# Kernel optimization log

Hardware: AMD Instinct MI355X
Metric: run time of the kernel (lower is better)

## Reference

```python
import jax, jax.numpy as jnp
import numpy as np
from jax import lax

B, T1, T2, C = 8, 128, 128, 256
K = 3

def setup_inputs() -> dict:
    key = jax.random.key(0)
    k1, k2, kw, kb = jax.random.split(key, 4)
    x1 = jax.random.normal(k1, (B, T1, C), dtype=jnp.float32)
    x2 = jax.random.normal(k2, (B, T2, C), dtype=jnp.float32)
    # conv2d: in_channels = 2C, out_channels = C, kernel 3x3 (OIHW)
    fan_in = 2 * C * K * K
    bound = 1.0 / np.sqrt(fan_in)
    W = jax.random.uniform(kw, (C, 2 * C, K, K), jnp.float32, -bound, bound)
    b = jax.random.uniform(kb, (C,), jnp.float32, -bound, bound)
    alpha = jnp.float32(0.5)
    return {"x1": x1, "x2": x2, "W": W, "b": b, "alpha": alpha}


def reference(x1, x2, W, b, alpha):
    # x1: [B, T1, C], x2: [B, T2, C]
    a = jnp.transpose(x1, (0, 2, 1))  # [B, C, T1]
    c2 = jnp.transpose(x2, (0, 2, 1))  # [B, C, T2]
    Bd, Cd, T1d = a.shape
    T2d = c2.shape[-1]
    # joint outer-product tensor: [B, 2C, T1, T2]
    j1 = jnp.broadcast_to(a[:, :, :, None], (Bd, Cd, T1d, T2d))
    j2 = jnp.broadcast_to(c2[:, :, None, :], (Bd, Cd, T1d, T2d))
    joint = jnp.concatenate([j1, j2], axis=1)
    out = lax.conv_general_dilated(
        joint, W, window_strides=(1, 1), padding="SAME",
        dimension_numbers=("NCHW", "OIHW", "NCHW"))
    out = out + b[None, :, None, None]
    out = jax.nn.gelu(out, approximate=False)  # torch nn.GELU default = exact erf
    out_T1 = jnp.mean(out, axis=-1)            # [B, C, T1]
    out_T1 = jnp.transpose(out_T1, (0, 2, 1))  # [B, T1, C]
    return out_T1 * alpha + x1
```

## Files before the change

kernel.cpp:

```cpp
#include <hip/hip_runtime.h>
#include <math.h>

#define B_   8
#define T_   128
#define C_   256
#define KP   768
#define NQ   768

typedef unsigned short ushort;
typedef ushort ushort4v __attribute__((ext_vector_type(4)));
typedef ushort ushort8v __attribute__((ext_vector_type(8)));
typedef __bf16 bf16x8  __attribute__((ext_vector_type(8)));
typedef float  f32x4   __attribute__((ext_vector_type(4)));

__device__ __forceinline__ ushort f2bf(float f) {
    unsigned u = __float_as_uint(f);
    u += 0x7fffu + ((u >> 16) & 1u);
    return (ushort)(u >> 16);
}

__device__ __forceinline__ float gelu_fast(float x) {
    float x2 = x * x;
    float y  = x * fmaf(0.0713548162726f, x2, 1.59576912161f);
    float e  = __expf(-y);
    return x * __builtin_amdgcn_rcpf(1.0f + e);
}

__global__ __launch_bounds__(256) void tc_pack(
    const float* __restrict__ x1, const float* __restrict__ x2,
    const float* __restrict__ W, ushort* __restrict__ Lmat,
    ushort* __restrict__ Wmat)
{
    const int bid = blockIdx.x, tid = threadIdx.x;
    if (bid < 1536) {
        int cid  = bid * 256 + tid;
        int pc   = cid % 192;
        int rest = cid / 192;
        int m    = rest & 127;
        int sb   = rest >> 7;
        int tap  = pc >> 6, ci = (pc & 63) * 4;
        const float* X = (sb >= 8 ? x2 + (size_t)(sb - 8) * T_ * C_
                                  : x1 + (size_t)sb * T_ * C_);
        int row = m + tap - 1;
        float4 v = make_float4(0.f, 0.f, 0.f, 0.f);
        if (row >= 0 && row < T_) v = *(const float4*)&X[row * C_ + ci];
        ushort4v u; u.x = f2bf(v.x); u.y = f2bf(v.y); u.z = f2bf(v.z); u.w = f2bf(v.w);
        *(ushort4v*)&Lmat[(size_t)cid * 4] = u;
    } else {
        int cid  = (bid - 1536) * 256 + tid;
        int pc   = cid % 192;
        int rest = cid / 192;
        int q    = rest % 768;
        int s    = rest / 768;
        int tap  = pc >> 6, ci = (pc & 63) * 4;
        int o    = q / 3;
        int r    = q - o * 3;
        ushort4v u;
        #pragma unroll
        for (int j = 0; j < 4; ++j) {
            int cj = ci + j;
            int addr = (s == 0) ? o * 4608 + cj * 9 + tap * 3 + r
                                : o * 4608 + (256 + cj) * 9 + r * 3 + tap;
            float w = W[addr];
            ushort b = f2bf(w);
            if (j == 0) u.x = b; else if (j == 1) u.y = b; else if (j == 2) u.z = b; else u.w = b;
        }
        *(ushort4v*)&Wmat[(size_t)cid * 4] = u;
    }
}

__global__ __launch_bounds__(256) void tc_mfma(
    const ushort* __restrict__ Lmat, const ushort* __restrict__ Wmat,
    float* __restrict__ Y)
{
    const int tile_n = blockIdx.x;
    const int tile_m = blockIdx.y;
    const int side   = blockIdx.z & 1;
    const int b      = blockIdx.z >> 1;

    __shared__ ushort As[64 * 40];
    __shared__ ushort Bs[64 * 40];

    const int tid = threadIdx.x;
    const int l   = tid & 63, w = tid >> 6;
    const int wr  = w >> 1,  wc = w & 1;
    const int r16 = l & 15,  kb = l >> 4;

    f32x4 acc[2][2] = {};

    const ushort* Lbase = Lmat + ((size_t)(side * B_ + b) * T_ + tile_m * 64 + (tid >> 2)) * KP + (tid & 3) * 8;
    const ushort* Wbase = Wmat + ((size_t)side * NQ + tile_n * 64 + (tid >> 2)) * KP + (tid & 3) * 8;
    const int aoff = (tid >> 2) * 40 + (tid & 3) * 8;

    const int ra = (wr * 32 + r16) * 40 + kb * 8;
    const int rb = (wc * 32 + r16) * 40 + kb * 8;

    ushort8v av = *(const ushort8v*)Lbase;
    ushort8v bv = *(const ushort8v*)Wbase;

    for (int k0 = 0; k0 < KP; k0 += 32) {
        __syncthreads();
        *(ushort8v*)&As[aoff] = av;
        *(ushort8v*)&Bs[aoff] = bv;
        __syncthreads();
        if (k0 < KP - 32) {
            av = *(const ushort8v*)(Lbase + k0 + 32);
            bv = *(const ushort8v*)(Wbase + k0 + 32);
        }
        bf16x8 a0 = __builtin_bit_cast(bf16x8, *(const ushort8v*)&As[ra]);
        bf16x8 a1 = __builtin_bit_cast(bf16x8, *(const ushort8v*)&As[ra + 16 * 40]);
        bf16x8 b0 = __builtin_bit_cast(bf16x8, *(const ushort8v*)&Bs[rb]);
        bf16x8 b1 = __builtin_bit_cast(bf16x8, *(const ushort8v*)&Bs[rb + 16 * 40]);
        acc[0][0] = __builtin_amdgcn_mfma_f32_16x16x32_bf16(a0, b0, acc[0][0], 0, 0, 0);
        acc[0][1] = __builtin_amdgcn_mfma_f32_16x16x32_bf16(a0, b1, acc[0][1], 0, 0, 0);
        acc[1][0] = __builtin_amdgcn_mfma_f32_16x16x32_bf16(a1, b0, acc[1][0], 0, 0, 0);
        acc[1][1] = __builtin_amdgcn_mfma_f32_16x16x32_bf16(a1, b1, acc[1][1], 0, 0, 0);
    }

    #pragma unroll
    for (int j = 0; j < 2; ++j) {
        int gq = tile_n * 64 + wc * 32 + j * 16 + r16;
        #pragma unroll
        for (int i = 0; i < 2; ++i) {
            int gm = tile_m * 64 + wr * 32 + i * 16 + kb * 4;
            float* p = Y + ((size_t)(side * B_ + b) * NQ + gq) * T_ + gm;
            *(f32x4*)p = acc[i][j];
        }
    }
}

__global__ __launch_bounds__(128) void tc_finalize(
    const float* __restrict__ Y, const float* __restrict__ x1,
    const float* __restrict__ bias, const float* __restrict__ alpha_p,
    float* __restrict__ out)
{
    const int o = blockIdx.x & 255;
    const int b = blockIdx.x >> 8;
    const int t = threadIdx.x;

    __shared__ float Bs3[T_], BsT[T_], BsB[T_];

    const float* YB = Y + ((size_t)(B_ + b) * NQ + o * 3) * T_ + t;
    float b0 = YB[0], b1 = YB[T_], b2 = YB[2 * T_];
    Bs3[t] = b0 + b1 + b2;
    BsT[t] = b1 + b2;
    BsB[t] = b0 + b1;

    const float* YA = Y + ((size_t)b * NQ + o * 3) * T_ + t;
    float a0 = YA[0], a1 = YA[T_], a2 = YA[2 * T_];
    float bo = bias[o];
    float A3 = bo + a0 + a1 + a2;
    float Al = bo + a1 + a2;
    float Ar = bo + a0 + a1;

    __syncthreads();

    const float* Bsel = (t == 0) ? BsT : ((t == T_ - 1) ? BsB : Bs3);

    float s0 = 0.f, s1 = 0.f, s2 = 0.f, s3 = 0.f;
    for (int j = 0; j < T_; j += 4) {
        s0 += gelu_fast(A3 + Bsel[j]);
        s1 += gelu_fast(A3 + Bsel[j + 1]);
        s2 += gelu_fast(A3 + Bsel[j + 2]);
        s3 += gelu_fast(A3 + Bsel[j + 3]);
    }
    float s = (s0 + s1) + (s2 + s3);
    s += gelu_fast(Al + Bsel[0])      - gelu_fast(A3 + Bsel[0]);
    s += gelu_fast(Ar + Bsel[T_ - 1]) - gelu_fast(A3 + Bsel[T_ - 1]);

    float alpha = *alpha_p;
    size_t oi = ((size_t)b * T_ + t) * C_ + o;
    out[oi] = s * (alpha * (1.0f / (float)T_)) + x1[oi];
}

extern "C" void kernel_launch(void* const* d_in, const int* in_sizes, int n_in,
                              void* d_out, int out_size, void* d_ws, size_t ws_size,
                              hipStream_t stream) {
    const float* x1    = (const float*)d_in[0];
    const float* x2    = (const float*)d_in[1];
    const float* W     = (const float*)d_in[2];
    const float* bias  = (const float*)d_in[3];
    const float* alpha = (const float*)d_in[4];
    float* out = (float*)d_out;

    float*  Y    = (float*)d_ws;
    ushort* Lmat = (ushort*)((char*)d_ws + (size_t)2 * B_ * NQ * T_ * 4);
    ushort* Wmat = Lmat + (size_t)2 * B_ * T_ * KP;

    tc_pack<<<1536 + 1152, 256, 0, stream>>>(x1, x2, W, Lmat, Wmat);
    tc_mfma<<<dim3(NQ / 64, T_ / 64, 2 * B_), 256, 0, stream>>>(Lmat, Wmat, Y);
    tc_finalize<<<B_ * C_, T_, 0, stream>>>(Y, x1, bias, alpha, out);
}
```

Measured before the change: 97.05 us.

## Compute per-tap GEMM outputs with K=256 and apply conv shifts in finalize

Replaces the im2col-style packed input matrix (K=768 with shifted rows) with a plain GEMM over all 9 kernel taps: each output is computed per tap with K=C=256 directly from fp32 inputs converted to bf16 on the fly. The time shifts and tap sums move into the finalize kernel, which gathers nine tap results with boundary masks. This removes the input-packing pass and the strided weight gather, and uses a transposed weight pack through shared memory. The cost is a larger intermediate G tensor (2x2304x1024 floats) and more gathered loads in finalize.

```diff
diff --git a/kernel.cpp b/kernel.cpp
--- a/kernel.cpp
+++ b/kernel.cpp
@@ -4,11 +4,11 @@
 #define B_   8
 #define T_   128
 #define C_   256
-#define KP   768
-#define NQ   768
+#define M_   1024
+#define NO   2304
+#define LDP  136
 
 typedef unsigned short ushort;
-typedef ushort ushort4v __attribute__((ext_vector_type(4)));
 typedef ushort ushort8v __attribute__((ext_vector_type(8)));
 typedef __bf16 bf16x8  __attribute__((ext_vector_type(8)));
 typedef float  f32x4   __attribute__((ext_vector_type(4)));
@@ -26,111 +26,122 @@
     return x * __builtin_amdgcn_rcpf(1.0f + e);
 }
 
-__global__ __launch_bounds__(256) void tc_pack(
+__device__ __forceinline__ ushort8v pack8(float4 lo, float4 hi) {
+    ushort8v u;
+    u[0] = f2bf(lo.x); u[1] = f2bf(lo.y); u[2] = f2bf(lo.z); u[3] = f2bf(lo.w);
+    u[4] = f2bf(hi.x); u[5] = f2bf(hi.y); u[6] = f2bf(hi.z); u[7] = f2bf(hi.w);
+    return u;
+}
+
+__global__ __launch_bounds__(256) void tc_pack_w(
+    const float* __restrict__ W, ushort* __restrict__ Wt)
+{
+    const int o = blockIdx.x, t = threadIdx.x;
+    __shared__ ushort lw[4608];
+    const float* src = W + (size_t)o * 4608;
+    #pragma unroll
+    for (int i = 0; i < 18; ++i)
+        lw[t + i * 256] = f2bf(src[t + i * 256]);
+    __syncthreads();
+    #pragma unroll
+    for (int i = 0; i < 18; ++i) {
+        int e   = t + i * 256;
+        int row = e >> 8;
+        int c   = e & 255;
+        int s   = (row >= 9);
+        int r   = row - s * 9;
+        Wt[((size_t)s * NO + o * 9 + r) * C_ + c] = lw[((s << 8) + c) * 9 + r];
+    }
+}
+
+__global__ __launch_bounds__(256) void tc_gemm(
     const float* __restrict__ x1, const float* __restrict__ x2,
-    const float* __restrict__ W, ushort* __restrict__ Lmat,
-    ushort* __restrict__ Wmat)
+    const ushort* __restrict__ Wt, float* __restrict__ G)
 {
-    const int bid = blockIdx.x, tid = threadIdx.x;
-    if (bid < 1536) {
-        int cid  = bid * 256 + tid;
-        int pc   = cid % 192;
-        int rest = cid / 192;
-        int m    = rest & 127;
-        int sb   = rest >> 7;
-        int tap  = pc >> 6, ci = (pc & 63) * 4;
-        const float* X = (sb >= 8 ? x2 + (size_t)(sb - 8) * T_ * C_
-                                  : x1 + (size_t)sb * T_ * C_);
-        int row = m + tap - 1;
-        float4 v = make_float4(0.f, 0.f, 0.f, 0.f);
-        if (row >= 0 && row < T_) v = *(const float4*)&X[row * C_ + ci];
-        ushort4v u; u.x = f2bf(v.x); u.y = f2bf(v.y); u.z = f2bf(v.z); u.w = f2bf(v.w);
-        *(ushort4v*)&Lmat[(size_t)cid * 4] = u;
-    } else {
-        int cid  = (bid - 1536) * 256 + tid;
-        int pc   = cid % 192;
-        int rest = cid / 192;
-        int q    = rest % 768;
-        int s    = rest / 768;
-        int tap  = pc >> 6, ci = (pc & 63) * 4;
-        int o    = q / 3;
-        int r    = q - o * 3;
-        ushort4v u;
-        #pragma unroll
-        for (int j = 0; j < 4; ++j) {
-            int cj = ci + j;
-            int addr = (s == 0) ? o * 4608 + cj * 9 + tap * 3 + r
-                                : o * 4608 + (256 + cj) * 9 + r * 3 + tap;
-            float w = W[addr];
-            ushort b = f2bf(w);
-            if (j == 0) u.x = b; else if (j == 1) u.y = b; else if (j == 2) u.z = b; else u.w = b;
-        }
-        *(ushort4v*)&Wmat[(size_t)cid * 4] = u;
-    }
-}
-
-__global__ __launch_bounds__(256) void tc_mfma(
-    const ushort* __restrict__ Lmat, const ushort* __restrict__ Wmat,
-    float* __restrict__ Y)
-{
-    const int tile_n = blockIdx.x;
-    const int tile_m = blockIdx.y;
-    const int side   = blockIdx.z & 1;
-    const int b      = blockIdx.z >> 1;
-
-    __shared__ ushort As[64 * 40];
-    __shared__ ushort Bs[64 * 40];
+    const int tn = blockIdx.x;
+    const int tm = blockIdx.y;
+    const int s  = blockIdx.z;
+
+    __shared__ ushort As[64 * LDP];
+    __shared__ ushort Bs[64 * LDP];
 
     const int tid = threadIdx.x;
-    const int l   = tid & 63, w = tid >> 6;
-    const int wr  = w >> 1,  wc = w & 1;
-    const int r16 = l & 15,  kb = l >> 4;
+    const int r   = tid & 63;
+    const int q   = tid >> 6;
+
+    const float*  Xr = (s ? x2 : x1) + ((size_t)(tm * 64 + r)) * C_ + q * 32;
+    const ushort* Wr = Wt + ((size_t)s * NO + tn * 64 + r) * C_ + q * 32;
+
+    float4 al0[8], al1[8];
+    ushort8v bl0[4], bl1[4];
+    #pragma unroll
+    for (int i = 0; i < 8; ++i) al0[i] = *(const float4*)(Xr + i * 4);
+    #pragma unroll
+    for (int i = 0; i < 4; ++i) bl0[i] = *(const ushort8v*)(Wr + i * 8);
+    #pragma unroll
+    for (int i = 0; i < 8; ++i) al1[i] = *(const float4*)(Xr + 128 + i * 4);
+    #pragma unroll
+    for (int i = 0; i < 4; ++i) bl1[i] = *(const ushort8v*)(Wr + 128 + i * 8);
+
+    const int st = r * LDP + q * 32;
+    #pragma unroll
+    for (int c = 0; c < 4; ++c) {
+        *(ushort8v*)&As[st + c * 8] = pack8(al0[2 * c], al0[2 * c + 1]);
+        *(ushort8v*)&Bs[st + c * 8] = bl0[c];
+    }
+    __syncthreads();
+
+    const int wr  = q >> 1, wc = q & 1;
+    const int r16 = tid & 15, kb = (tid & 63) >> 4;
+    const int ar  = (wr * 32 + r16) * LDP + kb * 8;
+    const int br  = (wc * 32 + r16) * LDP + kb * 8;
 
     f32x4 acc[2][2] = {};
-
-    const ushort* Lbase = Lmat + ((size_t)(side * B_ + b) * T_ + tile_m * 64 + (tid >> 2)) * KP + (tid & 3) * 8;
-    const ushort* Wbase = Wmat + ((size_t)side * NQ + tile_n * 64 + (tid >> 2)) * KP + (tid & 3) * 8;
-    const int aoff = (tid >> 2) * 40 + (tid & 3) * 8;
-
-    const int ra = (wr * 32 + r16) * 40 + kb * 8;
-    const int rb = (wc * 32 + r16) * 40 + kb * 8;
-
-    ushort8v av = *(const ushort8v*)Lbase;
-    ushort8v bv = *(const ushort8v*)Wbase;
-
-    for (int k0 = 0; k0 < KP; k0 += 32) {
-        __syncthreads();
-        *(ushort8v*)&As[aoff] = av;
-        *(ushort8v*)&Bs[aoff] = bv;
-        __syncthreads();
-        if (k0 < KP - 32) {
-            av = *(const ushort8v*)(Lbase + k0 + 32);
-            bv = *(const ushort8v*)(Wbase + k0 + 32);
-        }
-        bf16x8 a0 = __builtin_bit_cast(bf16x8, *(const ushort8v*)&As[ra]);
-        bf16x8 a1 = __builtin_bit_cast(bf16x8, *(const ushort8v*)&As[ra + 16 * 40]);
-        bf16x8 b0 = __builtin_bit_cast(bf16x8, *(const ushort8v*)&Bs[rb]);
-        bf16x8 b1 = __builtin_bit_cast(bf16x8, *(const ushort8v*)&Bs[rb + 16 * 40]);
+    #pragma unroll
+    for (int ks = 0; ks < 4; ++ks) {
+        bf16x8 a0 = __builtin_bit_cast(bf16x8, *(const ushort8v*)&As[ar + ks * 32]);
+        bf16x8 a1 = __builtin_bit_cast(bf16x8, *(const ushort8v*)&As[ar + 16 * LDP + ks * 32]);
+        bf16x8 b0 = __builtin_bit_cast(bf16x8, *(const ushort8v*)&Bs[br + ks * 32]);
+        bf16x8 b1 = __builtin_bit_cast(bf16x8, *(const ushort8v*)&Bs[br + 16 * LDP + ks * 32]);
         acc[0][0] = __builtin_amdgcn_mfma_f32_16x16x32_bf16(a0, b0, acc[0][0], 0, 0, 0);
         acc[0][1] = __builtin_amdgcn_mfma_f32_16x16x32_bf16(a0, b1, acc[0][1], 0, 0, 0);
         acc[1][0] = __builtin_amdgcn_mfma_f32_16x16x32_bf16(a1, b0, acc[1][0], 0, 0, 0);
         acc[1][1] = __builtin_amdgcn_mfma_f32_16x16x32_bf16(a1, b1, acc[1][1], 0, 0, 0);
     }
+    __syncthreads();
+
+    #pragma unroll
+    for (int c = 0; c < 4; ++c) {
+        *(ushort8v*)&As[st + c * 8] = pack8(al1[2 * c], al1[2 * c + 1]);
+        *(ushort8v*)&Bs[st + c * 8] = bl1[c];
+    }
+    __syncthreads();
+
+    #pragma unroll
+    for (int ks = 0; ks < 4; ++ks) {
+        bf16x8 a0 = __builtin_bit_cast(bf16x8, *(const ushort8v*)&As[ar + ks * 32]);
+        bf16x8 a1 = __builtin_bit_cast(bf16x8, *(const ushort8v*)&As[ar + 16 * LDP + ks * 32]);
+        bf16x8 b0 = __builtin_bit_cast(bf16x8, *(const ushort8v*)&Bs[br + ks * 32]);
+        bf16x8 b1 = __builtin_bit_cast(bf16x8, *(const ushort8v*)&Bs[br + 16 * LDP + ks * 32]);
+        acc[0][0] = __builtin_amdgcn_mfma_f32_16x16x32_bf16(a0, b0, acc[0][0], 0, 0, 0);
+        acc[0][1] = __builtin_amdgcn_mfma_f32_16x16x32_bf16(a0, b1, acc[0][1], 0, 0, 0);
+        acc[1][0] = __builtin_amdgcn_mfma_f32_16x16x32_bf16(a1, b0, acc[1][0], 0, 0, 0);
+        acc[1][1] = __builtin_amdgcn_mfma_f32_16x16x32_bf16(a1, b1, acc[1][1], 0, 0, 0);
+    }
 
     #pragma unroll
     for (int j = 0; j < 2; ++j) {
-        int gq = tile_n * 64 + wc * 32 + j * 16 + r16;
+        int n = tn * 64 + wc * 32 + j * 16 + r16;
         #pragma unroll
         for (int i = 0; i < 2; ++i) {
-            int gm = tile_m * 64 + wr * 32 + i * 16 + kb * 4;
-            float* p = Y + ((size_t)(side * B_ + b) * NQ + gq) * T_ + gm;
-            *(f32x4*)p = acc[i][j];
+            int m = tm * 64 + wr * 32 + i * 16 + kb * 4;
+            *(f32x4*)&G[((size_t)s * NO + n) * M_ + m] = acc[i][j];
         }
     }
 }
 
 __global__ __launch_bounds__(128) void tc_finalize(
-    const float* __restrict__ Y, const float* __restrict__ x1,
+    const float* __restrict__ G, const float* __restrict__ x1,
     const float* __restrict__ bias, const float* __restrict__ alpha_p,
     float* __restrict__ out)
 {
@@ -140,18 +151,38 @@
 
     __shared__ float Bs3[T_], BsT[T_], BsB[T_];
 
-    const float* YB = Y + ((size_t)(B_ + b) * NQ + o * 3) * T_ + t;
-    float b0 = YB[0], b1 = YB[T_], b2 = YB[2 * T_];
-    Bs3[t] = b0 + b1 + b2;
-    BsT[t] = b1 + b2;
-    BsB[t] = b0 + b1;
-
-    const float* YA = Y + ((size_t)b * NQ + o * 3) * T_ + t;
-    float a0 = YA[0], a1 = YA[T_], a2 = YA[2 * T_];
+    const float* G0 = G + ((size_t)o * 9) * M_ + b * T_;
+    const float* G1 = G + ((size_t)NO + o * 9) * M_ + b * T_;
+
+    float a[3] = {0.f, 0.f, 0.f};
+    #pragma unroll
+    for (int kh = 0; kh < 3; ++kh) {
+        int tm = t + kh - 1;
+        if (tm >= 0 && tm < T_) {
+            #pragma unroll
+            for (int kw = 0; kw < 3; ++kw)
+                a[kw] += G0[(kh * 3 + kw) * M_ + tm];
+        }
+    }
+    float bb[3] = {0.f, 0.f, 0.f};
+    #pragma unroll
+    for (int kw = 0; kw < 3; ++kw) {
+        int tm = t + kw - 1;
+        if (tm >= 0 && tm < T_) {
+            #pragma unroll
+            for (int kh = 0; kh < 3; ++kh)
+                bb[kh] += G1[(kh * 3 + kw) * M_ + tm];
+        }
+    }
+
+    Bs3[t] = bb[0] + bb[1] + bb[2];
+    BsT[t] = bb[1] + bb[2];
+    BsB[t] = bb[0] + bb[1];
+
     float bo = bias[o];
-    float A3 = bo + a0 + a1 + a2;
-    float Al = bo + a1 + a2;
-    float Ar = bo + a0 + a1;
+    float A3 = bo + a[0] + a[1] + a[2];
+    float Al = bo + a[1] + a[2];
+    float Ar = bo + a[0] + a[1];
 
     __syncthreads();
 
@@ -164,13 +195,13 @@
         s2 += gelu_fast(A3 + Bsel[j + 2]);
         s3 += gelu_fast(A3 + Bsel[j + 3]);
     }
-    float s = (s0 + s1) + (s2 + s3);
-    s += gelu_fast(Al + Bsel[0])      - gelu_fast(A3 + Bsel[0]);
-    s += gelu_fast(Ar + Bsel[T_ - 1]) - gelu_fast(A3 + Bsel[T_ - 1]);
+    float sacc = (s0 + s1) + (s2 + s3);
+    sacc += gelu_fast(Al + Bsel[0])      - gelu_fast(A3 + Bsel[0]);
+    sacc += gelu_fast(Ar + Bsel[T_ - 1]) - gelu_fast(A3 + Bsel[T_ - 1]);
 
     float alpha = *alpha_p;
     size_t oi = ((size_t)b * T_ + t) * C_ + o;
-    out[oi] = s * (alpha * (1.0f / (float)T_)) + x1[oi];
+    out[oi] = sacc * (alpha * (1.0f / (float)T_)) + x1[oi];
 }
 
 extern "C" void kernel_launch(void* const* d_in, const int* in_sizes, int n_in,
@@ -183,11 +214,10 @@
     const float* alpha = (const float*)d_in[4];
     float* out = (float*)d_out;
 
-    float*  Y    = (float*)d_ws;
-    ushort* Lmat = (ushort*)((char*)d_ws + (size_t)2 * B_ * NQ * T_ * 4);
-    ushort* Wmat = Lmat + (size_t)2 * B_ * T_ * KP;
-
-    tc_pack<<<1536 + 1152, 256, 0, stream>>>(x1, x2, W, Lmat, Wmat);
-    tc_mfma<<<dim3(NQ / 64, T_ / 64, 2 * B_), 256, 0, stream>>>(Lmat, Wmat, Y);
-    tc_finalize<<<B_ * C_, T_, 0, stream>>>(Y, x1, bias, alpha, out);
-}
+    float*  G  = (float*)d_ws;
+    ushort* Wt = (ushort*)((char*)d_ws + (size_t)2 * NO * M_ * 4);
+
+    tc_pack_w<<<256, 256, 0, stream>>>(W, Wt);
+    tc_gemm<<<dim3(NO / 64, M_ / 64, 2), 256, 0, stream>>>(x1, x2, Wt, G);
+    tc_finalize<<<B_ * C_, T_, 0, stream>>>(G, x1, bias, alpha, out);
+}
```

Result: slower. 104.6 us (+7.8%).
